# Performance work log

Measured on AMD Instinct MI355X. Metric: run time of the kernel, lower is better.

The kernel has to match this reference:

```python
import jax, jax.numpy as jnp
import numpy as np

IN_DIM = 1024
HID = 2048
BATCH = 8192


def setup_inputs() -> dict:
    key = jax.random.key(0)
    ks = jax.random.split(key, 10)
    s1 = 1.0 / np.sqrt(IN_DIM)
    s2 = 1.0 / np.sqrt(HID)
    inp = {
        "x": jax.random.normal(ks[0], (BATCH, IN_DIM), dtype=jnp.float32),
        "W1": jax.random.uniform(ks[1], (IN_DIM, HID), jnp.float32, -s1, s1),
        "b1": jax.random.uniform(ks[2], (HID,), jnp.float32, -s1, s1),
        "W2": jax.random.uniform(ks[3], (HID, HID), jnp.float32, -s2, s2),
        "b2": jax.random.uniform(ks[4], (HID,), jnp.float32, -s2, s2),
        "W3": jax.random.uniform(ks[5], (HID, HID), jnp.float32, -s2, s2),
        "b3": jax.random.uniform(ks[6], (HID,), jnp.float32, -s2, s2),
        "Wout": jax.random.uniform(ks[7], (HID, 1), jnp.float32, -s2, s2),
        "bout": jax.random.uniform(ks[8], (1,), jnp.float32, -s2, s2),
        "weight": jnp.array([0.1], dtype=jnp.float32),
        "bias": jnp.array([0.0], dtype=jnp.float32),
        "scale": jnp.array([1.0], dtype=jnp.float32),
        "shift": jnp.array([0.0], dtype=jnp.float32),
    }
    return inp


def reference(x, W1, b1, W2, b2, W3, b3, Wout, bout, weight, bias, scale, shift):
    # 3-layer tanh MLP core
    h = jnp.tanh(x @ W1 + b1)
    h = jnp.tanh(h @ W2 + b2)
    core_out = jnp.tanh(h @ W3 + b3)  # [B, HID]
    # Closed form of per-element 1-qubit statevector sim:
    # <Y> for RX(w) RY(v) H |0>  ==  sin(w) * sin(v)
    q_out = jnp.sin(weight[0]) * jnp.sin(core_out)
    q_out = (q_out + bias[0]) * scale[0] + shift[0]
    out = core_out + q_out
    out = out @ Wout + bout  # [B, 1]
    return out.squeeze(-1)  # [B]
```

## Files before the change

kernel.cpp:

```cpp
#include <hip/hip_runtime.h>
#include <hip/hip_bf16.h>


typedef _Float16 f16;
typedef __attribute__((ext_vector_type(8))) _Float16 f16x8;
typedef __attribute__((ext_vector_type(4))) _Float16 f16x4;
typedef __attribute__((ext_vector_type(4))) float f32x4;

#define BATCH 8192
#define IN_DIM 1024
#define HID 2048

__device__ __forceinline__ float fast_tanh(float x) {
  x = fminf(12.0f, fmaxf(-12.0f, x));
  float e = __expf(2.0f * x);
  return (e - 1.0f) * __builtin_amdgcn_rcpf(e + 1.0f);
}

__global__ __launch_bounds__(256) void cast_kernel(const float* __restrict__ in,
                                                   f16* __restrict__ out, int n4) {
  int i = blockIdx.x * blockDim.x + threadIdx.x;
  if (i < n4) {
    float4 v = reinterpret_cast<const float4*>(in)[i];
    f16x4 o = { (f16)v.x, (f16)v.y, (f16)v.z, (f16)v.w };
    reinterpret_cast<f16x4*>(out)[i] = o;
  }
}

__global__ __launch_bounds__(256) void transpose_cast_kernel(const float* __restrict__ W,
                                                             f16* __restrict__ Wt,
                                                             int K, int N) {
  __shared__ float tile[32][33];
  int kb = blockIdx.y * 32, nb = blockIdx.x * 32;
  int tx = threadIdx.x, ty = threadIdx.y;
#pragma unroll
  for (int i = 0; i < 4; ++i)
    tile[ty + i * 8][tx] = W[(size_t)(kb + ty + i * 8) * N + nb + tx];
  __syncthreads();
#pragma unroll
  for (int i = 0; i < 4; ++i)
    Wt[(size_t)(nb + ty + i * 8) * K + kb + tx] = (f16)tile[tx][ty + i * 8];
}

#define GLDS16(g, l)                                                         \
  __builtin_amdgcn_global_load_lds(                                          \
      (const __attribute__((address_space(1))) unsigned int*)(g),            \
      (__attribute__((address_space(3))) unsigned int*)(l), 16, 0, 0)

__global__ __launch_bounds__(256) void gemm_bias_tanh(
    const f16* __restrict__ A,
    const f16* __restrict__ Bt,
    const float* __restrict__ bias,
    f16* __restrict__ Out,
    int K) {
  __shared__ f16 As[128 * 64];
  __shared__ f16 Bs[128 * 64];

  const int t = threadIdx.x;
  const int l = t & 63;
  const int w = t >> 6;
  const int wr = w >> 1, wc = w & 1;
  const int bm = (int)blockIdx.x >> 4;
  const int bn = (int)blockIdx.x & 15;
  const int tm = bm << 7, tn = bn << 7;

  const int lr = l & 15;
  const int lk = (l >> 4) << 3;

  const int se = t * 8;
  const int sm = se >> 6;
  const int sk = se & 63;
  const int wbase = w * 512;

  f32x4 acc[4][4] = {};

  for (int k0 = 0; k0 < K; k0 += 64) {
    const f16* ga = A  + (size_t)(tm + sm) * K + k0 + sk;
    const f16* gb = Bt + (size_t)(tn + sm) * K + k0 + sk;
#pragma unroll
    for (int r = 0; r < 4; ++r)
      GLDS16(ga + (size_t)(r * 32) * K, &As[r * 2048 + wbase]);
#pragma unroll
    for (int r = 0; r < 4; ++r)
      GLDS16(gb + (size_t)(r * 32) * K, &Bs[r * 2048 + wbase]);
    __syncthreads();

#pragma unroll
    for (int ks = 0; ks < 2; ++ks) {
      f16x8 af[4], bf[4];
#pragma unroll
      for (int mi = 0; mi < 4; ++mi)
        af[mi] = *reinterpret_cast<const f16x8*>(
            &As[(wr * 64 + mi * 16 + lr) * 64 + ks * 32 + lk]);
#pragma unroll
      for (int ni = 0; ni < 4; ++ni)
        bf[ni] = *reinterpret_cast<const f16x8*>(
            &Bs[(wc * 64 + ni * 16 + lr) * 64 + ks * 32 + lk]);
#pragma unroll
      for (int mi = 0; mi < 4; ++mi)
#pragma unroll
        for (int ni = 0; ni < 4; ++ni)
          acc[mi][ni] = __builtin_amdgcn_mfma_f32_16x16x32_f16(
              af[mi], bf[ni], acc[mi][ni], 0, 0, 0);
    }
    __syncthreads();
  }

#pragma unroll
  for (int ni = 0; ni < 4; ++ni) {
    int col = tn + wc * 64 + ni * 16 + lr;
    float bv = bias[col];
#pragma unroll
    for (int mi = 0; mi < 4; ++mi) {
      int row0 = tm + wr * 64 + mi * 16 + ((l >> 4) << 2);
#pragma unroll
      for (int j = 0; j < 4; ++j) {
        float v = fast_tanh(acc[mi][ni][j] + bv);
        Out[(size_t)(row0 + j) * HID + col] = (f16)v;
      }
    }
  }
}

__global__ __launch_bounds__(256) void final_reduce(
    const f16* __restrict__ core, const float* __restrict__ Wout,
    const float* __restrict__ bout, const float* __restrict__ weight,
    const float* __restrict__ qbias, const float* __restrict__ qscale,
    const float* __restrict__ qshift, float* __restrict__ out) {
  const int b = blockIdx.x, t = threadIdx.x;
  const float sw = __sinf(weight[0]);
  const float qb = qbias[0], qs = qscale[0], qsh = qshift[0];
  f16x8 c8 = *reinterpret_cast<const f16x8*>(&core[(size_t)b * HID + t * 8]);
  float sum = 0.f;
#pragma unroll
  for (int j = 0; j < 8; ++j) {
    float c = (float)c8[j];
    float s = c + (sw * __sinf(c) + qb) * qs + qsh;
    sum += s * Wout[t * 8 + j];
  }
#pragma unroll
  for (int off = 32; off >= 1; off >>= 1) sum += __shfl_down(sum, off, 64);
  __shared__ float red[4];
  if ((t & 63) == 0) red[t >> 6] = sum;
  __syncthreads();
  if (t == 0) out[b] = red[0] + red[1] + red[2] + red[3] + bout[0];
}

extern "C" void kernel_launch(void* const* d_in, const int* in_sizes, int n_in,
                              void* d_out, int out_size, void* d_ws, size_t ws_size,
                              hipStream_t stream) {
  const float* x    = (const float*)d_in[0];
  const float* W1   = (const float*)d_in[1];
  const float* b1   = (const float*)d_in[2];
  const float* W2   = (const float*)d_in[3];
  const float* b2   = (const float*)d_in[4];
  const float* W3   = (const float*)d_in[5];
  const float* b3   = (const float*)d_in[6];
  const float* Wout = (const float*)d_in[7];
  const float* bout = (const float*)d_in[8];
  const float* wgt  = (const float*)d_in[9];
  const float* qb   = (const float*)d_in[10];
  const float* qs   = (const float*)d_in[11];
  const float* qsh  = (const float*)d_in[12];
  float* out = (float*)d_out;

  char* ws = (char*)d_ws;
  size_t off = 0;
  f16* xh  = (f16*)(ws + off); off += (size_t)BATCH * IN_DIM * sizeof(f16);
  f16* w1t = (f16*)(ws + off); off += (size_t)HID * IN_DIM * sizeof(f16);
  f16* w2t = (f16*)(ws + off); off += (size_t)HID * HID * sizeof(f16);
  f16* w3t = (f16*)(ws + off); off += (size_t)HID * HID * sizeof(f16);
  f16* h1  = (f16*)(ws + off); off += (size_t)BATCH * HID * sizeof(f16);
  f16* h2  = (f16*)(ws + off); off += (size_t)BATCH * HID * sizeof(f16);

  {
    int n4 = BATCH * IN_DIM / 4;
    cast_kernel<<<(n4 + 255) / 256, 256, 0, stream>>>(x, xh, n4);
  }
  {
    dim3 blk(32, 8);
    transpose_cast_kernel<<<dim3(HID / 32, IN_DIM / 32), blk, 0, stream>>>(W1, w1t, IN_DIM, HID);
    transpose_cast_kernel<<<dim3(HID / 32, HID / 32),    blk, 0, stream>>>(W2, w2t, HID, HID);
    transpose_cast_kernel<<<dim3(HID / 32, HID / 32),    blk, 0, stream>>>(W3, w3t, HID, HID);
  }
  const int grid = (BATCH / 128) * (HID / 128);
  gemm_bias_tanh<<<grid, 256, 0, stream>>>(xh, w1t, b1, h1, IN_DIM);
  gemm_bias_tanh<<<grid, 256, 0, stream>>>(h1, w2t, b2, h2, HID);
  gemm_bias_tanh<<<grid, 256, 0, stream>>>(h2, w3t, b3, h1, HID);
  final_reduce<<<BATCH, 256, 0, stream>>>(h1, Wout, bout, wgt, qb, qs, qsh, out);
}
```

Measured before the change: 392.7 us.

## Rewrite GEMM as 256x256 tile with 4-stage LDS ring and ping-pong MFMA

Replaces the 128x128, 256-thread GEMM with a 256x256, 512-thread kernel templated on K. It uses a 4-deep LDS ring with K-steps of 32, prefetched two steps ahead. Barriers split each step into two MFMA halves and raise priority around them, so global-to-LDS loads overlap with compute. The larger tile halves global traffic per FLOP and the explicit waitcnt/barrier schedule aims to hide load latency. The costs are 64KB of LDS per block and heavier register pressure, which limit occupancy, and a hand-tuned sync scheme that is fragile.

```diff
diff --git a/kernel.cpp b/kernel.cpp
--- a/kernel.cpp
+++ b/kernel.cpp
@@ -42,77 +42,123 @@
     Wt[(size_t)(nb + ty + i * 8) * K + kb + tx] = (f16)tile[tx][ty + i * 8];
 }
 
+
 #define GLDS16(g, l)                                                         \
   __builtin_amdgcn_global_load_lds(                                          \
       (const __attribute__((address_space(1))) unsigned int*)(g),            \
       (__attribute__((address_space(3))) unsigned int*)(l), 16, 0, 0)
 
-__global__ __launch_bounds__(256) void gemm_bias_tanh(
+template <int K>
+__global__ __launch_bounds__(512, 2) void gemm256_bias_tanh(
     const f16* __restrict__ A,
     const f16* __restrict__ Bt,
     const float* __restrict__ bias,
-    f16* __restrict__ Out,
-    int K) {
-  __shared__ f16 As[128 * 64];
-  __shared__ f16 Bs[128 * 64];
-
-  const int t = threadIdx.x;
-  const int l = t & 63;
-  const int w = t >> 6;
-  const int wr = w >> 1, wc = w & 1;
-  const int bm = (int)blockIdx.x >> 4;
-  const int bn = (int)blockIdx.x & 15;
-  const int tm = bm << 7, tn = bn << 7;
-
+    f16* __restrict__ Out) {
+  constexpr int NT = K / 32;
+  __shared__ f16 As[4][8192];
+  __shared__ f16 Bs[4][8192];
+
+  const int T = threadIdx.x;
+  const int l = T & 63;
+  const int w = T >> 6;
+  const int wm = w >> 2, wn = w & 3;
   const int lr = l & 15;
-  const int lk = (l >> 4) << 3;
-
-  const int se = t * 8;
-  const int sm = se >> 6;
-  const int sk = se & 63;
-  const int wbase = w * 512;
-
-  f32x4 acc[4][4] = {};
-
-  for (int k0 = 0; k0 < K; k0 += 64) {
-    const f16* ga = A  + (size_t)(tm + sm) * K + k0 + sk;
-    const f16* gb = Bt + (size_t)(tn + sm) * K + k0 + sk;
-#pragma unroll
-    for (int r = 0; r < 4; ++r)
-      GLDS16(ga + (size_t)(r * 32) * K, &As[r * 2048 + wbase]);
-#pragma unroll
-    for (int r = 0; r < 4; ++r)
-      GLDS16(gb + (size_t)(r * 32) * K, &Bs[r * 2048 + wbase]);
-    __syncthreads();
-
-#pragma unroll
-    for (int ks = 0; ks < 2; ++ks) {
-      f16x8 af[4], bf[4];
-#pragma unroll
-      for (int mi = 0; mi < 4; ++mi)
-        af[mi] = *reinterpret_cast<const f16x8*>(
-            &As[(wr * 64 + mi * 16 + lr) * 64 + ks * 32 + lk]);
+  const int lc = l >> 4;
+
+  const int bm = (int)blockIdx.x >> 3;
+  const int bn = (int)blockIdx.x & 7;
+  const int tm = bm << 8, tn = bn << 8;
+
+  const int srow = ((T >> 5) << 3) + (T & 7);
+  const int skel = ((T >> 3) & 3) << 3;
+  const f16* gA0 = A + (size_t)(tm + srow) * K + skel;
+  const f16* gA1 = A + (size_t)(tm + srow + 128) * K + skel;
+  const f16* gB0 = Bt + (size_t)(tn + srow) * K + skel;
+  const f16* gB1 = Bt + (size_t)(tn + srow + 128) * K + skel;
+  const int ldsw0 = w * 512;
+  const int ldsw1 = 4096 + w * 512;
+
+  const int abase = (wm * 16 + (lr >> 3)) * 256 + lc * 64 + (lr & 7) * 8;
+  const int bbase = (wn * 8 + (lr >> 3)) * 256 + lc * 64 + (lr & 7) * 8;
+
+  f32x4 acc[8][4] = {};
+
+  GLDS16(gA0, &As[0][ldsw0]);
+  GLDS16(gA1, &As[0][ldsw1]);
+  GLDS16(gB0, &Bs[0][ldsw0]);
+  GLDS16(gB1, &Bs[0][ldsw1]);
+  GLDS16(gA0 + 32, &As[1][ldsw0]);
+  GLDS16(gA1 + 32, &As[1][ldsw1]);
+  GLDS16(gB0 + 32, &Bs[1][ldsw0]);
+  GLDS16(gB1 + 32, &Bs[1][ldsw1]);
+  asm volatile("s_waitcnt vmcnt(4)" ::: "memory");
+  __builtin_amdgcn_s_barrier();
+  __builtin_amdgcn_sched_barrier(0);
+
+  for (int t = 0; t < NT; ++t) {
+    const int q = t & 3;
+    f16x8 afr[4], bfr[4];
+#pragma unroll
+    for (int mi = 0; mi < 4; ++mi)
+      afr[mi] = *reinterpret_cast<const f16x8*>(&As[q][abase + mi * 512]);
+#pragma unroll
+    for (int ni = 0; ni < 4; ++ni)
+      bfr[ni] = *reinterpret_cast<const f16x8*>(&Bs[q][bbase + ni * 512]);
+    if (t + 2 < NT) {
+      const int q2 = (t + 2) & 3;
+      const int ko = (t + 2) * 32;
+      GLDS16(gA0 + ko, &As[q2][ldsw0]);
+      GLDS16(gA1 + ko, &As[q2][ldsw1]);
+    }
+    __builtin_amdgcn_s_barrier();
+    asm volatile("s_waitcnt lgkmcnt(0)" ::: "memory");
+    __builtin_amdgcn_sched_barrier(0);
+    __builtin_amdgcn_s_setprio(1);
+#pragma unroll
+    for (int mi = 0; mi < 4; ++mi)
 #pragma unroll
       for (int ni = 0; ni < 4; ++ni)
-        bf[ni] = *reinterpret_cast<const f16x8*>(
-            &Bs[(wc * 64 + ni * 16 + lr) * 64 + ks * 32 + lk]);
-#pragma unroll
-      for (int mi = 0; mi < 4; ++mi)
-#pragma unroll
-        for (int ni = 0; ni < 4; ++ni)
-          acc[mi][ni] = __builtin_amdgcn_mfma_f32_16x16x32_f16(
-              af[mi], bf[ni], acc[mi][ni], 0, 0, 0);
+        acc[mi][ni] = __builtin_amdgcn_mfma_f32_16x16x32_f16(
+            afr[mi], bfr[ni], acc[mi][ni], 0, 0, 0);
+    __builtin_amdgcn_s_setprio(0);
+    __builtin_amdgcn_s_barrier();
+    __builtin_amdgcn_sched_barrier(0);
+
+    f16x8 afr2[4];
+#pragma unroll
+    for (int mi = 0; mi < 4; ++mi)
+      afr2[mi] = *reinterpret_cast<const f16x8*>(&As[q][abase + (4 + mi) * 512]);
+    if (t + 2 < NT) {
+      const int q2 = (t + 2) & 3;
+      const int ko = (t + 2) * 32;
+      GLDS16(gB0 + ko, &Bs[q2][ldsw0]);
+      GLDS16(gB1 + ko, &Bs[q2][ldsw1]);
+      asm volatile("s_waitcnt vmcnt(4)" ::: "memory");
+    } else {
+      asm volatile("s_waitcnt vmcnt(0)" ::: "memory");
     }
-    __syncthreads();
+    __builtin_amdgcn_s_barrier();
+    asm volatile("s_waitcnt lgkmcnt(0)" ::: "memory");
+    __builtin_amdgcn_sched_barrier(0);
+    __builtin_amdgcn_s_setprio(1);
+#pragma unroll
+    for (int mi = 0; mi < 4; ++mi)
+#pragma unroll
+      for (int ni = 0; ni < 4; ++ni)
+        acc[4 + mi][ni] = __builtin_amdgcn_mfma_f32_16x16x32_f16(
+            afr2[mi], bfr[ni], acc[4 + mi][ni], 0, 0, 0);
+    __builtin_amdgcn_s_setprio(0);
+    __builtin_amdgcn_s_barrier();
+    __builtin_amdgcn_sched_barrier(0);
   }
 
 #pragma unroll
   for (int ni = 0; ni < 4; ++ni) {
-    int col = tn + wc * 64 + ni * 16 + lr;
-    float bv = bias[col];
-#pragma unroll
-    for (int mi = 0; mi < 4; ++mi) {
-      int row0 = tm + wr * 64 + mi * 16 + ((l >> 4) << 2);
+    const int col = tn + wn * 64 + ni * 16 + lr;
+    const float bv = bias[col];
+#pragma unroll
+    for (int mi = 0; mi < 8; ++mi) {
+      const int row0 = tm + wm * 128 + mi * 16 + ((l >> 4) << 2);
 #pragma unroll
       for (int j = 0; j < 4; ++j) {
         float v = fast_tanh(acc[mi][ni][j] + bv);
@@ -183,9 +229,9 @@
     transpose_cast_kernel<<<dim3(HID / 32, HID / 32),    blk, 0, stream>>>(W2, w2t, HID, HID);
     transpose_cast_kernel<<<dim3(HID / 32, HID / 32),    blk, 0, stream>>>(W3, w3t, HID, HID);
   }
-  const int grid = (BATCH / 128) * (HID / 128);
-  gemm_bias_tanh<<<grid, 256, 0, stream>>>(xh, w1t, b1, h1, IN_DIM);
-  gemm_bias_tanh<<<grid, 256, 0, stream>>>(h1, w2t, b2, h2, HID);
-  gemm_bias_tanh<<<grid, 256, 0, stream>>>(h2, w3t, b3, h1, HID);
+  const int grid = (BATCH / 256) * (HID / 256);
+  gemm256_bias_tanh<IN_DIM><<<grid, 512, 0, stream>>>(xh, w1t, b1, h1);
+  gemm256_bias_tanh<HID>   <<<grid, 512, 0, stream>>>(h1, w2t, b2, h2);
+  gemm256_bias_tanh<HID>   <<<grid, 512, 0, stream>>>(h2, w3t, b3, h1);
   final_reduce<<<BATCH, 256, 0, stream>>>(h1, Wout, bout, wgt, qb, qs, qsh, out);
 }
```

After: 362.2 us. 1.08x faster.
